# Performance work log

Measured on AMD Instinct MI355X. Metric: run time of the kernel, lower is better.

Reference implementation:

```python
import jax, jax.numpy as jnp
import numpy as np

B, T, D = 16, 4096, 1024
HID = 4 * D // 3  # 1365, per SelectorMLP(hidden=4*d//3)
RHO, TAU, LN_EPS = 0.2, 1.0, 1e-5


def setup_inputs() -> dict:
    key = jax.random.key(0)
    ks = jax.random.split(key, 6)
    embeddings = jax.random.normal(ks[0], (B, T, D), dtype=jnp.float32)
    attn = (jax.random.uniform(ks[1], (B, T)) < 0.9).astype(jnp.float32)
    ln_w = jnp.ones((D,), jnp.float32)
    ln_b = jnp.zeros((D,), jnp.float32)
    fc1_w = jax.random.normal(ks[2], (HID, D), jnp.float32) * (1.0 / np.sqrt(D))
    fc1_b = jnp.zeros((HID,), jnp.float32)
    fc2_w = jax.random.normal(ks[3], (1, HID), jnp.float32) * (1.0 / np.sqrt(HID))
    fc2_b = jnp.zeros((1,), jnp.float32)
    return {"embeddings": embeddings, "attn": attn, "ln_w": ln_w, "ln_b": ln_b,
            "fc1_w": fc1_w, "fc1_b": fc1_b, "fc2_w": fc2_w, "fc2_b": fc2_b}


def _hard_topk(z, K):
    # z: [B,T], K: [B,1] float integer budgets -> exact top-K 0/1 mask per row
    b, t = z.shape
    order = jnp.argsort(-z, axis=1)                       # descending sort indices
    mask = (jnp.arange(t)[None, :] < K).astype(z.dtype)   # [B,T] first-K ranks
    h = jnp.zeros_like(z).at[jnp.arange(b)[:, None], order].set(mask)
    return h


def reference(embeddings, attn, ln_w, ln_b, fc1_w, fc1_b, fc2_w, fc2_b):
    emb = embeddings * attn[:, :, None]                    # [B,T,D]
    # SelectorMLP (dropout = identity in eval)
    mu = jnp.mean(emb, axis=-1, keepdims=True)
    var = jnp.mean(jnp.square(emb - mu), axis=-1, keepdims=True)
    x = (emb - mu) / jnp.sqrt(var + LN_EPS) * ln_w + ln_b
    x = jax.nn.gelu(jnp.einsum('btd,hd->bth', x, fc1_w) + fc1_b, approximate=False)
    scores = jnp.einsum('bth,oh->bto', x, fc2_w)[..., 0] + fc2_b[0]  # [B,T]
    scores = jnp.where(attn == 0, -1e9, scores)
    p = jax.nn.softmax(scores / TAU, axis=1)
    entropy = -jnp.sum(p * jnp.log(p + 1e-12), axis=1)     # [B]
    T_eff = jnp.clip(jnp.sum(attn, axis=1), 1, None)
    norm_entropy = jnp.mean(entropy / jnp.log(T_eff))
    T_eff2 = jnp.sum(attn, axis=1, keepdims=True)          # [B,1]
    K = jnp.clip(jnp.round(RHO * T_eff2), 1, None)
    z = K * p
    h = _hard_topk(z, K)
    g = h + (z - jax.lax.stop_gradient(z))                 # straight-through
    return g, z, norm_entropy
```

## Files before the change

### kernel.cpp

```cpp
#include <hip/hip_runtime.h>
#include <math.h>

#define B_ 16
#define T_ 4096
#define D_ 1024
#define HID_ 1365
#define NPAD 1408
#define NGRP 88
#define N_TOK (B_*T_)
#define RHO_ 0.2f
#define LN_EPS_ 1e-5f
#define SC 1024.0f
#define INV_SC2 (1.0f/(1024.0f*1024.0f))

#define NHT 11
#define WCHUNKS (NGRP*32*4*16)
#define NG16 4096
#define ACHUNKS ((size_t)NG16*32*64)

typedef _Float16 f16x8 __attribute__((ext_vector_type(8)));
typedef float f32x4 __attribute__((ext_vector_type(4)));

__device__ __forceinline__ void gl16(const void* g, void* l) {
  __builtin_amdgcn_global_load_lds(
      (const __attribute__((address_space(1))) unsigned int*)g,
      (__attribute__((address_space(3))) unsigned int*)l, 16, 0, 0);
}

__global__ __launch_bounds__(256) void wsplit_kernel(
    const float* __restrict__ fc1w, f16x8* __restrict__ whi, f16x8* __restrict__ wlo)
{
  int c = blockIdx.x * 256 + threadIdx.x;
  if (c >= WCHUNKS) return;
  int ln = c & 15, q = (c >> 4) & 3, ks = (c >> 6) & 31, g = c >> 11;
  int n = g * 16 + ln;
  int k = ks * 32 + q * 8;
  f16x8 hi, lo;
#pragma unroll
  for (int j = 0; j < 8; ++j) {
    float v = (n < HID_) ? fc1w[(size_t)n * D_ + k + j] * SC : 0.f;
    _Float16 h = (_Float16)v;
    hi[j] = h;
    lo[j] = (_Float16)(v - (float)h);
  }
  whi[c] = hi;
  wlo[c] = lo;
}

#define FSTR 1028
__global__ __launch_bounds__(256, 2) void lnasplit_kernel(
    const float* __restrict__ emb, const float* __restrict__ attn,
    const float* __restrict__ lnw, const float* __restrict__ lnb,
    f16x8* __restrict__ ahi, f16x8* __restrict__ alo)
{
  __shared__ float tile[16 * FSTR];
  __shared__ float smu[16], srs[16];
  int tid = threadIdx.x;
  int g = blockIdx.x;
  int wave = tid >> 6, lane = tid & 63;
#pragma unroll
  for (int it = 0; it < 16; ++it) {
    int idx = tid + it * 256;
    int row = idx >> 8, c4 = idx & 255;
    float a = attn[g * 16 + row];
    float4 v = *reinterpret_cast<const float4*>(
        emb + (size_t)(g * 16 + row) * D_ + c4 * 4);
    v.x *= a; v.y *= a; v.z *= a; v.w *= a;
    *reinterpret_cast<float4*>(&tile[row * FSTR + c4 * 4]) = v;
  }
  __syncthreads();
#pragma unroll
  for (int r4 = 0; r4 < 4; ++r4) {
    int row = wave * 4 + r4;
    float s = 0.f, sq = 0.f;
#pragma unroll
    for (int q = 0; q < 4; ++q) {
      float4 v = *reinterpret_cast<const float4*>(&tile[row * FSTR + lane * 4 + q * 256]);
      s  += v.x + v.y + v.z + v.w;
      sq += v.x * v.x + v.y * v.y + v.z * v.z + v.w * v.w;
    }
#pragma unroll
    for (int off = 32; off > 0; off >>= 1) {
      s  += __shfl_down(s, off, 64);
      sq += __shfl_down(sq, off, 64);
    }
    if (lane == 0) {
      float m = s * (1.f / D_);
      float var = sq * (1.f / D_) - m * m;
      if (var < 0.f) var = 0.f;
      smu[row] = m;
      srs[row] = 1.f / sqrtf(var + LN_EPS_);
    }
  }
  __syncthreads();
#pragma unroll
  for (int it = 0; it < 8; ++it) {
    int idx = tid + it * 256;
    int ksl = idx >> 6, l = idx & 63;
    int ln = l & 15, q = l >> 4;
    float rs = srs[ln];
    float nmr = -smu[ln] * rs;
    int colbase = ksl * 32 + q * 8;
    float4 e0 = *reinterpret_cast<const float4*>(&tile[ln * FSTR + colbase]);
    float4 e1 = *reinterpret_cast<const float4*>(&tile[ln * FSTR + colbase + 4]);
    float ev[8] = {e0.x, e0.y, e0.z, e0.w, e1.x, e1.y, e1.z, e1.w};
    f16x8 hi, lo;
#pragma unroll
    for (int j = 0; j < 8; ++j) {
      int kg = colbase + j;
      float wv = lnw[kg], bv = lnb[kg];
      float y = fmaf(ev[j] * rs, wv, fmaf(nmr, wv, bv)) * SC;
      _Float16 h = (_Float16)y;
      hi[j] = h;
      lo[j] = (_Float16)(y - (float)h);
    }
    size_t c = (size_t)(g * 32 + ksl) * 64 + l;
    ahi[c] = hi;
    alo[c] = lo;
  }
}

__global__ __launch_bounds__(512, 2) void mfma_score_v7(
    const f16x8* __restrict__ ahi, const f16x8* __restrict__ alo,
    const f16x8* __restrict__ whi, const f16x8* __restrict__ wlo,
    const float* __restrict__ fc1b, const float* __restrict__ fc2w,
    float* __restrict__ partial)
{
  __shared__ f16x8 sbuf[2][3072];
  __shared__ float red[2][256];
  int tid = threadIdx.x, lane = tid & 63;
  int w = tid >> 6, wrow = w & 3, wcol = w >> 2;
  int flat = blockIdx.x;
  int xcd = flat & 7, j = flat >> 3;
  int tb = xcd * 32 + j / NHT;
  int ht = j % NHT;
  int g0 = tb * 16;
  int hb0 = ht * 8;
  int ln16 = lane & 15, quad = lane >> 4;

  int u0 = w * 6;
  const f16x8* sp[6];
#pragma unroll
  for (int i = 0; i < 6; ++i) {
    int u = u0 + i;
    const f16x8* base;
    int grp;
    if (u < 16)      { base = ahi; grp = g0 + u; }
    else if (u < 32) { base = alo; grp = g0 + (u - 16); }
    else if (u < 40) { base = whi; grp = hb0 + (u - 32); }
    else             { base = wlo; grp = hb0 + (u - 40); }
    sp[i] = base + (size_t)grp * 2048 + lane;
  }

#define PBAR() do { __builtin_amdgcn_sched_barrier(0); \
                    __builtin_amdgcn_s_barrier();      \
                    __builtin_amdgcn_sched_barrier(0); } while (0)
#define LG0()  do { asm volatile("s_waitcnt lgkmcnt(0)" ::: "memory"); \
                    __builtin_amdgcn_sched_barrier(0); } while (0)

  f32x4 acc[4][4];
#pragma unroll
  for (int i = 0; i < 4; ++i)
#pragma unroll
    for (int j2 = 0; j2 < 4; ++j2) acc[i][j2] = (f32x4)0.f;

#pragma unroll
  for (int i = 0; i < 6; ++i)
    gl16(sp[i], &sbuf[0][(u0 + i) * 64]);
  __builtin_amdgcn_sched_barrier(0);
  asm volatile("s_waitcnt vmcnt(0)" ::: "memory");
  __builtin_amdgcn_s_barrier();
  __builtin_amdgcn_sched_barrier(0);

#pragma unroll 1
  for (int ks = 0; ks < 32; ++ks) {
    int cur = ks & 1;
    const f16x8* sb = &sbuf[cur][0];
    f16x8* nb = &sbuf[cur ^ 1][0];

    f16x8 ah[4], bh[4];
#pragma unroll
    for (int mi = 0; mi < 4; ++mi) ah[mi] = sb[(wrow * 4 + mi) * 64 + lane];
#pragma unroll
    for (int nj = 0; nj < 4; ++nj) bh[nj] = sb[2048 + (wcol * 4 + nj) * 64 + lane];
    if (ks < 31) {
#pragma unroll
      for (int i = 0; i < 6; ++i)
        gl16(sp[i] + (size_t)(ks + 1) * 64, &nb[(u0 + i) * 64]);
    }
    PBAR();
    LG0();
    __builtin_amdgcn_s_setprio(1);
#pragma unroll
    for (int mi = 0; mi < 4; ++mi)
#pragma unroll
      for (int nj = 0; nj < 4; ++nj)
        acc[mi][nj] = __builtin_amdgcn_mfma_f32_16x16x32_f16(ah[mi], bh[nj], acc[mi][nj], 0, 0, 0);
    __builtin_amdgcn_s_setprio(0);
    PBAR();

    f16x8 al[4];
#pragma unroll
    for (int mi = 0; mi < 4; ++mi) al[mi] = sb[1024 + (wrow * 4 + mi) * 64 + lane];
    PBAR();
    LG0();
    __builtin_amdgcn_s_setprio(1);
#pragma unroll
    for (int mi = 0; mi < 4; ++mi)
#pragma unroll
      for (int nj = 0; nj < 4; ++nj)
        acc[mi][nj] = __builtin_amdgcn_mfma_f32_16x16x32_f16(al[mi], bh[nj], acc[mi][nj], 0, 0, 0);
    __builtin_amdgcn_s_setprio(0);
    PBAR();

    f16x8 bl[4];
#pragma unroll
    for (int nj = 0; nj < 4; ++nj) bl[nj] = sb[2560 + (wcol * 4 + nj) * 64 + lane];
    PBAR();
    LG0();
    __builtin_amdgcn_s_setprio(1);
#pragma unroll
    for (int mi = 0; mi < 4; ++mi)
#pragma unroll
      for (int nj = 0; nj < 4; ++nj)
        acc[mi][nj] = __builtin_amdgcn_mfma_f32_16x16x32_f16(ah[mi], bl[nj], acc[mi][nj], 0, 0, 0);
    __builtin_amdgcn_s_setprio(0);
    __builtin_amdgcn_sched_barrier(0);
    asm volatile("s_waitcnt vmcnt(0)" ::: "memory");
    __builtin_amdgcn_s_barrier();
    __builtin_amdgcn_sched_barrier(0);
  }

#undef PBAR
#undef LG0

  int gb0 = hb0 + wcol * 4;
  float s[4][4];
#pragma unroll
  for (int mi = 0; mi < 4; ++mi)
#pragma unroll
    for (int r = 0; r < 4; ++r) s[mi][r] = 0.f;
#pragma unroll
  for (int nj = 0; nj < 4; ++nj) {
    int h = (gb0 + nj) * 16 + ln16;
    float b1 = 0.f, w2 = 0.f;
    if (h < HID_) { b1 = fc1b[h]; w2 = fc2w[h]; }
#pragma unroll
    for (int mi = 0; mi < 4; ++mi)
#pragma unroll
      for (int r = 0; r < 4; ++r) {
        float v = acc[mi][nj][r] * INV_SC2 + b1;
        float gel = 0.5f * v * (1.f + erff(v * 0.70710678118654752440f));
        s[mi][r] = fmaf(gel, w2, s[mi][r]);
      }
  }
#pragma unroll
  for (int mi = 0; mi < 4; ++mi)
#pragma unroll
    for (int r = 0; r < 4; ++r) {
      float v = s[mi][r];
      v += __shfl_xor(v, 1, 64);
      v += __shfl_xor(v, 2, 64);
      v += __shfl_xor(v, 4, 64);
      v += __shfl_xor(v, 8, 64);
      s[mi][r] = v;
    }
  if (ln16 == 0) {
#pragma unroll
    for (int mi = 0; mi < 4; ++mi)
#pragma unroll
      for (int r = 0; r < 4; ++r)
        red[wcol][wrow * 64 + mi * 16 + quad * 4 + r] = s[mi][r];
  }
  __syncthreads();
  if (tid < 256)
    partial[(size_t)ht * N_TOK + tb * 256 + tid] = red[0][tid] + red[1][tid];
}

__global__ __launch_bounds__(1024) void softmax_kernel(
    const float* __restrict__ partial, const float* __restrict__ fc2b,
    const float* __restrict__ attn,
    float* __restrict__ out_z, float* __restrict__ rowent, float* __restrict__ rowK)
{
  __shared__ float buf[1024];
  int b = blockIdx.x, tid = threadIdx.x;
  const float* arow = attn + b * T_;
  float sv[4], av[4];
  float f2b = fc2b[0];
#pragma unroll
  for (int q = 0; q < 4; ++q) {
    int t = tid + q * 1024;
    av[q] = arow[t];
    float sc = f2b;
#pragma unroll
    for (int p = 0; p < NHT; ++p) sc += partial[(size_t)p * N_TOK + b * T_ + t];
    sv[q] = (av[q] == 0.f) ? -1e9f : sc;
  }
  float m = fmaxf(fmaxf(sv[0], sv[1]), fmaxf(sv[2], sv[3]));
  buf[tid] = m; __syncthreads();
  for (int s = 512; s > 0; s >>= 1) { if (tid < s) buf[tid] = fmaxf(buf[tid], buf[tid + s]); __syncthreads(); }
  m = buf[0]; __syncthreads();
  float e[4]; float es = 0.f, as = 0.f;
#pragma unroll
  for (int q = 0; q < 4; ++q) { e[q] = expf(sv[q] - m); es += e[q]; as += av[q]; }
  buf[tid] = es; __syncthreads();
  for (int s = 512; s > 0; s >>= 1) { if (tid < s) buf[tid] += buf[tid + s]; __syncthreads(); }
  es = buf[0]; __syncthreads();
  buf[tid] = as; __syncthreads();
  for (int s = 512; s > 0; s >>= 1) { if (tid < s) buf[tid] += buf[tid + s]; __syncthreads(); }
  as = buf[0]; __syncthreads();
  float K = fmaxf(1.f, rintf(RHO_ * as));
  float inv = 1.f / es;
  float ent = 0.f;
#pragma unroll
  for (int q = 0; q < 4; ++q) {
    float p = e[q] * inv;
    out_z[b * T_ + tid + q * 1024] = K * p;
    ent -= p * logf(p + 1e-12f);
  }
  buf[tid] = ent; __syncthreads();
  for (int s = 512; s > 0; s >>= 1) { if (tid < s) buf[tid] += buf[tid + s]; __syncthreads(); }
  if (tid == 0) {
    rowent[b] = buf[0] / logf(fmaxf(as, 1.f));
    rowK[b] = K;
  }
}

__global__ __launch_bounds__(1024) void topk_kernel(
    const float* __restrict__ zall, float* __restrict__ g,
    const float* __restrict__ rowent, const float* __restrict__ rowK,
    float* __restrict__ out_scalar)
{
  __shared__ unsigned hist[256];
  __shared__ unsigned s_prefix, s_kk;
  __shared__ int s_cgt, s_ceq;
  int b = blockIdx.x, tid = threadIdx.x;
  const float* zrow = zall + b * T_;
  unsigned zb[4];
#pragma unroll
  for (int q = 0; q < 4; ++q) zb[q] = __float_as_uint(zrow[tid + q * 1024]);
  int K = (int)rowK[b];

  unsigned prefix = 0;
  unsigned kk = (unsigned)K;
#pragma unroll
  for (int pass = 0; pass < 4; ++pass) {
    int sh = 24 - pass * 8;
    unsigned pmask = pass ? (0xFFFFFFFFu << (sh + 8)) : 0u;
    if (tid < 256) hist[tid] = 0;
    __syncthreads();
#pragma unroll
    for (int q = 0; q < 4; ++q) {
      unsigned v = zb[q];
      if ((v & pmask) == (prefix & pmask)) atomicAdd(&hist[(v >> sh) & 255], 1u);
    }
    __syncthreads();
    if (tid == 0) {
      unsigned acc = 0;
      int bsel = 0;
      for (int i = 255; i >= 0; --i) {
        unsigned c = hist[i];
        if (acc + c >= kk) { bsel = i; s_kk = kk - acc; break; }
        acc += c;
      }
      s_prefix = prefix | ((unsigned)bsel << sh);
    }
    __syncthreads();
    prefix = s_prefix; kk = s_kk;
    __syncthreads();
  }
  if (tid == 0) { s_cgt = 0; s_ceq = 0; }
  __syncthreads();
  int cg = 0, ce = 0;
#pragma unroll
  for (int q = 0; q < 4; ++q) {
    if (zb[q] > prefix) ++cg;
    else if (zb[q] == prefix) ++ce;
  }
  if (cg) atomicAdd(&s_cgt, cg);
  if (ce) atomicAdd(&s_ceq, ce);
  __syncthreads();
  int need = K - s_cgt;
  bool allEq = (s_ceq == need);
  float* grow = g + b * T_;
#pragma unroll
  for (int q = 0; q < 4; ++q) {
    int t = tid + q * 1024;
    unsigned v = zb[q];
    if (v > prefix) grow[t] = 1.f;
    else if (v < prefix) grow[t] = 0.f;
    else if (allEq) grow[t] = 1.f;
  }
  __syncthreads();
  if (!allEq && tid == 0) {
    int cnt = 0;
    for (int t = 0; t < T_; ++t) {
      if (__float_as_uint(zrow[t]) == prefix) { grow[t] = (cnt < need) ? 1.f : 0.f; ++cnt; }
    }
  }
  if (b == 0 && tid == 0) {
    float s = 0.f;
    for (int i = 0; i < B_; ++i) s += rowent[i];
    out_scalar[0] = s * (1.f / B_);
  }
}

extern "C" void kernel_launch(void* const* d_in, const int* in_sizes, int n_in,
                              void* d_out, int out_size, void* d_ws, size_t ws_size,
                              hipStream_t stream)
{
  const float* emb  = (const float*)d_in[0];
  const float* attn = (const float*)d_in[1];
  const float* lnw  = (const float*)d_in[2];
  const float* lnb  = (const float*)d_in[3];
  const float* fc1w = (const float*)d_in[4];
  const float* fc1b = (const float*)d_in[5];
  const float* fc2w = (const float*)d_in[6];
  const float* fc2b = (const float*)d_in[7];

  float* out = (float*)d_out;
  float* g  = out;
  float* z  = out + N_TOK;
  float* ns = out + 2 * N_TOK;

  float* mu      = (float*)d_ws;
  float* rstd    = mu + N_TOK;
  float* partial = rstd + N_TOK;
  float* rowent  = partial + (size_t)NHT * N_TOK;
  float* rowK    = rowent + 16;
  f16x8* whi     = (f16x8*)(rowK + 16);
  f16x8* wlo     = whi + WCHUNKS;
  f16x8* ahi     = wlo + WCHUNKS;
  f16x8* alo     = ahi + ACHUNKS;

  wsplit_kernel<<<(WCHUNKS + 255) / 256, 256, 0, stream>>>(fc1w, whi, wlo);
  lnasplit_kernel<<<NG16, 256, 0, stream>>>(emb, attn, lnw, lnb, ahi, alo);
  mfma_score_v7<<<8 * 32 * NHT, 512, 0, stream>>>(ahi, alo, whi, wlo, fc1b, fc2w, partial);
  softmax_kernel<<<B_, 1024, 0, stream>>>(partial, fc2b, attn, z, rowent, rowK);
  topk_kernel<<<B_, 1024, 0, stream>>>(z, g, rowent, rowK, ns);
}
```

Measured before the change: 1.150 ms.

## Replace LDS-staged GEMM with direct-to-register double-buffered loads in smaller blocks

The score GEMM no longer stages A/B tiles through LDS via global_load_lds with barriers. Each wave now loads its own fragments straight from global memory into two register sets (P/Q), ping-ponging between them to overlap loads with MFMAs. Blocks shrink from 512 to 256 threads covering 128 tokens each, with twice as many blocks. This removes LDS traffic and block-wide barriers, but it drops cross-wave sharing of A and B tiles, so global and L2 traffic per FLOP goes up and register pressure rises.

```diff
diff --git a/kernel.cpp b/kernel.cpp
--- a/kernel.cpp
+++ b/kernel.cpp
@@ -21,12 +21,6 @@
 typedef _Float16 f16x8 __attribute__((ext_vector_type(8)));
 typedef float f32x4 __attribute__((ext_vector_type(4)));
 
-__device__ __forceinline__ void gl16(const void* g, void* l) {
-  __builtin_amdgcn_global_load_lds(
-      (const __attribute__((address_space(1))) unsigned int*)g,
-      (__attribute__((address_space(3))) unsigned int*)l, 16, 0, 0);
-}
-
 __global__ __launch_bounds__(256) void wsplit_kernel(
     const float* __restrict__ fc1w, f16x8* __restrict__ whi, f16x8* __restrict__ wlo)
 {
@@ -120,43 +114,27 @@
   }
 }
 
-__global__ __launch_bounds__(512, 2) void mfma_score_v7(
+__global__ __launch_bounds__(256, 2) void mfma_score_v8(
     const f16x8* __restrict__ ahi, const f16x8* __restrict__ alo,
     const f16x8* __restrict__ whi, const f16x8* __restrict__ wlo,
     const float* __restrict__ fc1b, const float* __restrict__ fc2w,
     float* __restrict__ partial)
 {
-  __shared__ f16x8 sbuf[2][3072];
-  __shared__ float red[2][256];
+  __shared__ float red[2][128];
   int tid = threadIdx.x, lane = tid & 63;
-  int w = tid >> 6, wrow = w & 3, wcol = w >> 2;
+  int w = tid >> 6, wrow = w & 1, wcol = w >> 1;
   int flat = blockIdx.x;
   int xcd = flat & 7, j = flat >> 3;
-  int tb = xcd * 32 + j / NHT;
+  int tb = xcd * 64 + j / NHT;
   int ht = j % NHT;
-  int g0 = tb * 16;
-  int hb0 = ht * 8;
+  int g0 = tb * 8 + wrow * 4;
+  int gb0 = ht * 8 + wcol * 4;
   int ln16 = lane & 15, quad = lane >> 4;
 
-  int u0 = w * 6;
-  const f16x8* sp[6];
-#pragma unroll
-  for (int i = 0; i < 6; ++i) {
-    int u = u0 + i;
-    const f16x8* base;
-    int grp;
-    if (u < 16)      { base = ahi; grp = g0 + u; }
-    else if (u < 32) { base = alo; grp = g0 + (u - 16); }
-    else if (u < 40) { base = whi; grp = hb0 + (u - 32); }
-    else             { base = wlo; grp = hb0 + (u - 40); }
-    sp[i] = base + (size_t)grp * 2048 + lane;
-  }
-
-#define PBAR() do { __builtin_amdgcn_sched_barrier(0); \
-                    __builtin_amdgcn_s_barrier();      \
-                    __builtin_amdgcn_sched_barrier(0); } while (0)
-#define LG0()  do { asm volatile("s_waitcnt lgkmcnt(0)" ::: "memory"); \
-                    __builtin_amdgcn_sched_barrier(0); } while (0)
+  const f16x8* srcAh = ahi + (size_t)g0 * 2048 + lane;
+  const f16x8* srcAl = alo + (size_t)g0 * 2048 + lane;
+  const f16x8* srcBh = whi + (size_t)gb0 * 2048 + lane;
+  const f16x8* srcBl = wlo + (size_t)gb0 * 2048 + lane;
 
   f32x4 acc[4][4];
 #pragma unroll
@@ -164,77 +142,47 @@
 #pragma unroll
     for (int j2 = 0; j2 < 4; ++j2) acc[i][j2] = (f32x4)0.f;
 
-#pragma unroll
-  for (int i = 0; i < 6; ++i)
-    gl16(sp[i], &sbuf[0][(u0 + i) * 64]);
-  __builtin_amdgcn_sched_barrier(0);
-  asm volatile("s_waitcnt vmcnt(0)" ::: "memory");
-  __builtin_amdgcn_s_barrier();
-  __builtin_amdgcn_sched_barrier(0);
-
+  f16x8 Pah[4], Pal[4], Pbh[4], Pbl[4];
+  f16x8 Qah[4], Qal[4], Qbh[4], Qbl[4];
+
+#define LOADSET(S, KS)                                           \
+  do {                                                           \
+    _Pragma("unroll")                                            \
+    for (int mi = 0; mi < 4; ++mi) {                             \
+      S##ah[mi] = srcAh[(size_t)mi * 2048 + (size_t)(KS) * 64];  \
+      S##al[mi] = srcAl[(size_t)mi * 2048 + (size_t)(KS) * 64];  \
+    }                                                            \
+    _Pragma("unroll")                                            \
+    for (int nj = 0; nj < 4; ++nj) {                             \
+      S##bh[nj] = srcBh[(size_t)nj * 2048 + (size_t)(KS) * 64];  \
+      S##bl[nj] = srcBl[(size_t)nj * 2048 + (size_t)(KS) * 64];  \
+    }                                                            \
+  } while (0)
+
+#define MFMASET(S)                                               \
+  do {                                                           \
+    _Pragma("unroll")                                            \
+    for (int mi = 0; mi < 4; ++mi)                               \
+      _Pragma("unroll")                                          \
+      for (int nj = 0; nj < 4; ++nj) {                           \
+        acc[mi][nj] = __builtin_amdgcn_mfma_f32_16x16x32_f16(S##ah[mi], S##bh[nj], acc[mi][nj], 0, 0, 0); \
+        acc[mi][nj] = __builtin_amdgcn_mfma_f32_16x16x32_f16(S##al[mi], S##bh[nj], acc[mi][nj], 0, 0, 0); \
+        acc[mi][nj] = __builtin_amdgcn_mfma_f32_16x16x32_f16(S##ah[mi], S##bl[nj], acc[mi][nj], 0, 0, 0); \
+      }                                                          \
+  } while (0)
+
+  LOADSET(P, 0);
 #pragma unroll 1
-  for (int ks = 0; ks < 32; ++ks) {
-    int cur = ks & 1;
-    const f16x8* sb = &sbuf[cur][0];
-    f16x8* nb = &sbuf[cur ^ 1][0];
-
-    f16x8 ah[4], bh[4];
-#pragma unroll
-    for (int mi = 0; mi < 4; ++mi) ah[mi] = sb[(wrow * 4 + mi) * 64 + lane];
-#pragma unroll
-    for (int nj = 0; nj < 4; ++nj) bh[nj] = sb[2048 + (wcol * 4 + nj) * 64 + lane];
-    if (ks < 31) {
-#pragma unroll
-      for (int i = 0; i < 6; ++i)
-        gl16(sp[i] + (size_t)(ks + 1) * 64, &nb[(u0 + i) * 64]);
-    }
-    PBAR();
-    LG0();
-    __builtin_amdgcn_s_setprio(1);
-#pragma unroll
-    for (int mi = 0; mi < 4; ++mi)
-#pragma unroll
-      for (int nj = 0; nj < 4; ++nj)
-        acc[mi][nj] = __builtin_amdgcn_mfma_f32_16x16x32_f16(ah[mi], bh[nj], acc[mi][nj], 0, 0, 0);
-    __builtin_amdgcn_s_setprio(0);
-    PBAR();
-
-    f16x8 al[4];
-#pragma unroll
-    for (int mi = 0; mi < 4; ++mi) al[mi] = sb[1024 + (wrow * 4 + mi) * 64 + lane];
-    PBAR();
-    LG0();
-    __builtin_amdgcn_s_setprio(1);
-#pragma unroll
-    for (int mi = 0; mi < 4; ++mi)
-#pragma unroll
-      for (int nj = 0; nj < 4; ++nj)
-        acc[mi][nj] = __builtin_amdgcn_mfma_f32_16x16x32_f16(al[mi], bh[nj], acc[mi][nj], 0, 0, 0);
-    __builtin_amdgcn_s_setprio(0);
-    PBAR();
-
-    f16x8 bl[4];
-#pragma unroll
-    for (int nj = 0; nj < 4; ++nj) bl[nj] = sb[2560 + (wcol * 4 + nj) * 64 + lane];
-    PBAR();
-    LG0();
-    __builtin_amdgcn_s_setprio(1);
-#pragma unroll
-    for (int mi = 0; mi < 4; ++mi)
-#pragma unroll
-      for (int nj = 0; nj < 4; ++nj)
-        acc[mi][nj] = __builtin_amdgcn_mfma_f32_16x16x32_f16(ah[mi], bl[nj], acc[mi][nj], 0, 0, 0);
-    __builtin_amdgcn_s_setprio(0);
-    __builtin_amdgcn_sched_barrier(0);
-    asm volatile("s_waitcnt vmcnt(0)" ::: "memory");
-    __builtin_amdgcn_s_barrier();
-    __builtin_amdgcn_sched_barrier(0);
-  }
-
-#undef PBAR
-#undef LG0
-
-  int gb0 = hb0 + wcol * 4;
+  for (int ks = 0; ks < 32; ks += 2) {
+    LOADSET(Q, ks + 1);
+    MFMASET(P);
+    if (ks + 2 < 32) LOADSET(P, ks + 2);
+    MFMASET(Q);
+  }
+
+#undef LOADSET
+#undef MFMASET
+
   float s[4][4];
 #pragma unroll
   for (int mi = 0; mi < 4; ++mi)
@@ -273,8 +221,8 @@
         red[wcol][wrow * 64 + mi * 16 + quad * 4 + r] = s[mi][r];
   }
   __syncthreads();
-  if (tid < 256)
-    partial[(size_t)ht * N_TOK + tb * 256 + tid] = red[0][tid] + red[1][tid];
+  if (tid < 128)
+    partial[(size_t)ht * N_TOK + tb * 128 + tid] = red[0][tid] + red[1][tid];
 }
 
 __global__ __launch_bounds__(1024) void softmax_kernel(
@@ -435,7 +383,7 @@
 
   wsplit_kernel<<<(WCHUNKS + 255) / 256, 256, 0, stream>>>(fc1w, whi, wlo);
   lnasplit_kernel<<<NG16, 256, 0, stream>>>(emb, attn, lnw, lnb, ahi, alo);
-  mfma_score_v7<<<8 * 32 * NHT, 512, 0, stream>>>(ahi, alo, whi, wlo, fc1b, fc2w, partial);
+  mfma_score_v8<<<8 * 64 * NHT, 256, 0, stream>>>(ahi, alo, whi, wlo, fc1b, fc2w, partial);
   softmax_kernel<<<B_, 1024, 0, stream>>>(partial, fc2b, attn, z, rowent, rowK);
   topk_kernel<<<B_, 1024, 0, stream>>>(z, g, rowent, rowK, ns);
 }
```

After: 1.032 ms. -10.3%, faster.
